# Kernel optimization log

Measured on AMD Instinct MI355X. Metric: run time of the kernel, lower is better.

Reference implementation:

```python
import jax, jax.numpy as jnp
import numpy as np

N_NODES = 100000
N_EDGES = 1600000
EPS = 1e-5  # nn.BatchNorm1d default eps


def setup_inputs() -> dict:
    key = jax.random.key(0)
    ks = jax.random.split(key, 6)
    x = jax.random.normal(ks[0], (N_NODES, 11), dtype=jnp.float32)
    edge_index = jax.random.randint(ks[1], (2, N_EDGES), 0, N_NODES, dtype=jnp.int64)
    edge_weight = jax.random.uniform(ks[2], (N_EDGES,), dtype=jnp.float32)
    W1 = jax.random.normal(ks[3], (11, 64), dtype=jnp.float32) * 0.3
    b1 = jnp.zeros((64,), dtype=jnp.float32)
    gamma = jnp.ones((64,), dtype=jnp.float32)
    beta = jnp.zeros((64,), dtype=jnp.float32)
    W2 = jax.random.normal(ks[4], (64, 128), dtype=jnp.float32) * 0.125
    b2 = jnp.zeros((128,), dtype=jnp.float32)
    return {"x": x, "edge_index": edge_index, "edge_weight": edge_weight,
            "W1": W1, "b1": b1, "gamma": gamma, "beta": beta, "W2": W2, "b2": b2}


def _gcn_conv(x, row, col, w, W, b, n_nodes):
    """PyG GCNConv: h = x @ W; symmetric-norm aggregate at col; + bias.
    row/col/w already include self loops (weight 1.0)."""
    h = x @ W  # [N, F_out]
    deg = jax.ops.segment_sum(w, col, num_segments=n_nodes)  # [N]
    dinv = jnp.where(deg > 0, jax.lax.rsqrt(jnp.maximum(deg, 1e-12)), 0.0)
    norm = dinv[row] * w * dinv[col]  # [E+N]
    msg = h[row] * norm[:, None]  # gather + scale, [E+N, F_out]
    out = jax.ops.segment_sum(msg, col, num_segments=n_nodes)  # scatter-add
    return out + b


def _batch_norm(x, gamma, beta):
    # training-mode BatchNorm1d over node dimension, biased variance
    mean = jnp.mean(x, axis=0)
    var = jnp.mean(jnp.square(x - mean), axis=0)
    return (x - mean) * jax.lax.rsqrt(var + EPS) * gamma + beta


def reference(x, edge_index, edge_weight, W1, b1, gamma, beta, W2, b2):
    n = x.shape[0]
    loops = jnp.arange(n, dtype=edge_index.dtype)
    row = jnp.concatenate([edge_index[0], loops])
    col = jnp.concatenate([edge_index[1], loops])
    w = jnp.concatenate([edge_weight, jnp.ones((n,), dtype=edge_weight.dtype)])

    h = _gcn_conv(x, row, col, w, W1, b1, n)
    h = _batch_norm(h, gamma, beta)
    h = jax.nn.relu(h)
    # dropout is identity at inference (deterministic baseline)
    out = _gcn_conv(h, row, col, w, W2, b2, n)
    return out
```

## Files before the change

kernel.cpp:

```cpp
#include <hip/hip_runtime.h>

#define F0 11
#define F1 64
#define F2 128
#define TN2 128

#define CHUNKS 64
#define BPR 12544
#define WPR (BPR / 2)
#define NBKT (CHUNKS * 8 * 4)
#define NN1 64

__device__ __forceinline__ unsigned short f2bf(float v) {
  unsigned u = __float_as_uint(v);
  unsigned r = u + 0x7FFFu + ((u >> 16) & 1u);
  return (unsigned short)(r >> 16);
}
__device__ __forceinline__ float bf2f(unsigned short s) {
  return __uint_as_float(((unsigned)s) << 16);
}
__device__ __forceinline__ float bf2f_lo(unsigned v) { return __uint_as_float(v << 16); }
__device__ __forceinline__ float bf2f_hi(unsigned v) { return __uint_as_float(v & 0xFFFF0000u); }

__global__ void k_pad(const float* __restrict__ x, unsigned short* __restrict__ x16b,
                      float* __restrict__ wdeg, int n) {
  int i = blockIdx.x * blockDim.x + threadIdx.x;
  if (i < n) wdeg[i] = 0.f;
  if (i >= n * 16) return;
  int r = i >> 4, f = i & 15;
  x16b[i] = (f < F0) ? f2bf(x[(size_t)r * F0 + f]) : (unsigned short)0;
}

__global__ __launch_bounds__(1024) void k_cnt8(const int* __restrict__ col,
                                               int* __restrict__ bcnt, int E, int CE) {
  __shared__ int scnt[16][8];
  int bid = blockIdx.x;
  int c = bid >> 2, q = bid & 3;
  int e0 = c * CE, e1 = min(E, e0 + CE);
  int S = (CE + 3) >> 2;
  int s0 = e0 + q * S, s1 = min(e1, s0 + S);
  int t = threadIdx.x, wv = t >> 6, lane = t & 63;
  int cr[8] = {0, 0, 0, 0, 0, 0, 0, 0};
  for (int e = s0 + t; e < s1; e += 1024) {
    int r = col[e] / BPR;
#pragma unroll
    for (int rr = 0; rr < 8; rr++) cr[rr] += (r == rr) ? 1 : 0;
  }
#pragma unroll
  for (int rr = 0; rr < 8; rr++) {
    int v = cr[rr];
#pragma unroll
    for (int d = 32; d > 0; d >>= 1) v += __shfl_down(v, d);
    if (lane == 0) scnt[wv][rr] = v;
  }
  __syncthreads();
  if (t < 8) {
    int s = 0;
    for (int i = 0; i < 16; i++) s += scnt[i][t];
    bcnt[(c * 8 + t) * 4 + q] = s;
  }
}

__global__ void k_scan8(const int* __restrict__ bcnt, int* __restrict__ boff) {
  __shared__ int s[1024];
  int t = threadIdx.x;
  int v0 = bcnt[2 * t], v1 = bcnt[2 * t + 1];
  int pv = v0 + v1;
  s[t] = pv;
  __syncthreads();
  for (int d = 1; d < 1024; d <<= 1) {
    int x = (t >= d) ? s[t - d] : 0;
    __syncthreads();
    s[t] += x;
    __syncthreads();
  }
  int ex = s[t] - pv;
  boff[2 * t] = ex;
  boff[2 * t + 1] = ex + v0;
  if (t == 1023) boff[2048] = s[1023];
}

__global__ __launch_bounds__(1024) void k_scatter(const int* __restrict__ col,
                                                  const int* __restrict__ row,
                                                  const float* __restrict__ w,
                                                  const int* __restrict__ boff,
                                                  unsigned short* __restrict__ bloc,
                                                  uint2* __restrict__ brw, int E, int CE) {
  __shared__ int cur[8];
  int bid = blockIdx.x;
  int c = bid >> 2, q = bid & 3;
  int t = threadIdx.x;
  if (t < 8) cur[t] = boff[(c * 8 + t) * 4 + q];
  __syncthreads();
  int e0 = c * CE, e1 = min(E, e0 + CE);
  int S = (CE + 3) >> 2;
  int s0 = e0 + q * S, s1 = min(e1, s0 + S);
  for (int e = s0 + t; e < s1; e += 1024) {
    int b = col[e];
    int r = b / BPR;
    int pos = atomicAdd(&cur[r], 1);
    bloc[pos] = (unsigned short)(b - r * BPR);
    brw[pos] = make_uint2((unsigned)row[e], __float_as_uint(w[e]));
  }
}

__global__ __launch_bounds__(1024) void k_hist2(const unsigned short* __restrict__ bloc,
                                                const uint2* __restrict__ brw,
                                                const int* __restrict__ boff,
                                                unsigned* __restrict__ partial,
                                                float* __restrict__ wdeg,
                                                int N, int ranges) {
  __shared__ unsigned lds[WPR];
  __shared__ float swdeg[BPR];
  int r = blockIdx.x % ranges;
  int c = blockIdx.x / ranges;
  int t = threadIdx.x;
  for (int i = t; i < WPR; i += 1024) lds[i] = 0;
  for (int i = t; i < BPR; i += 1024) swdeg[i] = 0.f;
  __syncthreads();
  int s0 = boff[(c * 8 + r) * 4], s1 = boff[(c * 8 + r) * 4 + 4];
  for (int i = s0 + t; i < s1; i += 1024) {
    int local = bloc[i];
    float wv = __uint_as_float(brw[i].y);
    atomicAdd(&lds[local >> 1], 1u << (16 * (local & 1)));
    atomicAdd(&swdeg[local], wv);
  }
  __syncthreads();
  unsigned* dst = partial + ((size_t)r * CHUNKS + c) * WPR;
  for (int i = t; i < WPR; i += 1024) dst[i] = lds[i];
  int lo = r * BPR;
  int hi = min(N, lo + BPR);
  for (int i = lo + t; i < hi; i += 1024) {
    float v = swdeg[i - lo];
    if (v != 0.f) atomicAdd(&wdeg[i], v);
  }
}

__global__ void k_dinv(const float* __restrict__ wdeg, float* __restrict__ dinv, int n) {
  int i = blockIdx.x * blockDim.x + threadIdx.x;
  if (i < n) dinv[i] = rsqrtf(1.0f + wdeg[i]);
}

__global__ void k_colprefix(const unsigned* __restrict__ partial,
                            unsigned short* __restrict__ rel,
                            int* __restrict__ cnt, int N, int npad) {
  int bin = blockIdx.x * blockDim.x + threadIdx.x;
  if (bin >= N) return;
  int r = bin / BPR, local = bin % BPR;
  int word = local >> 1, sh = 16 * (local & 1);
  const unsigned* p = partial + (size_t)r * CHUNKS * WPR + word;
  unsigned acc = 0;
  for (int c = 0; c < CHUNKS; c++) {
    unsigned v = (p[(size_t)c * WPR] >> sh) & 0xFFFFu;
    rel[(size_t)c * npad + bin] = (unsigned short)acc;
    acc += v;
  }
  cnt[bin] = (int)acc;
}

__global__ void k_scan1(const int* __restrict__ cnt, int* __restrict__ offs,
                        int* __restrict__ bsum, int n) {
  __shared__ int s[1024];
  int tid = threadIdx.x;
  int i = blockIdx.x * 1024 + tid;
  int v = (i < n) ? cnt[i] : 0;
  s[tid] = v;
  __syncthreads();
  for (int d = 1; d < 1024; d <<= 1) {
    int t = (tid >= d) ? s[tid - d] : 0;
    __syncthreads();
    s[tid] += t;
    __syncthreads();
  }
  if (i < n) offs[i] = s[tid] - v;
  if (tid == 1023) bsum[blockIdx.x] = s[1023];
}

__global__ void k_scan2(int* __restrict__ bsum, int nb) {
  __shared__ int s[256];
  __shared__ int carry;
  int t = threadIdx.x;
  if (t == 0) carry = 0;
  __syncthreads();
  for (int base = 0; base < nb; base += 256) {
    int v = (base + t < nb) ? bsum[base + t] : 0;
    s[t] = v;
    __syncthreads();
    for (int d = 1; d < 256; d <<= 1) {
      int x = (t >= d) ? s[t - d] : 0;
      __syncthreads();
      s[t] += x;
      __syncthreads();
    }
    int total = s[255];
    if (base + t < nb) bsum[base + t] = carry + s[t] - v;
    __syncthreads();
    if (t == 0) carry += total;
    __syncthreads();
  }
}

__global__ void k_scan3(int* __restrict__ offs, const int* __restrict__ bsum,
                        int n, int total) {
  int i = blockIdx.x * 1024 + threadIdx.x;
  if (i < n) offs[i] += bsum[blockIdx.x];
  if (i == 0) offs[n] = total;
}

__global__ __launch_bounds__(1024) void k_fill2(const unsigned short* __restrict__ bloc,
                                                const uint2* __restrict__ brw,
                                                const int* __restrict__ boff,
                                                const int* __restrict__ offs,
                                                const unsigned short* __restrict__ rel,
                                                const float* __restrict__ dinv,
                                                uint2* __restrict__ csr8,
                                                int N, int npad, int ranges) {
  __shared__ unsigned cur[WPR];
  int r = blockIdx.x % ranges;
  int c = blockIdx.x / ranges;
  int lo = r * BPR;
  int hi = min(N, lo + BPR);
  int t = threadIdx.x;
  const unsigned* rsrc = (const unsigned*)(rel + (size_t)c * npad + lo);
  int nw = (hi - lo + 1) >> 1;
  for (int i = t; i < nw; i += 1024) cur[i] = rsrc[i];
  __syncthreads();
  int s0 = boff[(c * 8 + r) * 4], s1 = boff[(c * 8 + r) * 4 + 4];
  for (int i = s0 + t; i < s1; i += 1024) {
    int local = bloc[i];
    int sh = 16 * (local & 1);
    unsigned old = atomicAdd(&cur[local >> 1], 1u << sh);
    unsigned myrel = (old >> sh) & 0xFFFFu;
    int pos = offs[lo + local] + (int)myrel;
    uint2 b = brw[i];
    float nm = dinv[b.x] * __uint_as_float(b.y);
    csr8[pos] = make_uint2(b.x | ((unsigned)local << 17), __float_as_uint(nm));
  }
}

__global__ __launch_bounds__(256) void k_agg1e(const unsigned short* __restrict__ x16b,
                                               const int* __restrict__ offs,
                                               const uint2* __restrict__ csr8,
                                               const float* __restrict__ dinv,
                                               const float* __restrict__ W1,
                                               const float* __restrict__ b1,
                                               unsigned short* __restrict__ h,
                                               float2* __restrict__ pbn, int N) {
  __shared__ float Ws[F0 * F1];
  __shared__ float bs[F1];
  __shared__ float sacc[NN1 * 16];
  __shared__ unsigned short sx[NN1 * 16];
  __shared__ float sdinv[NN1];
  __shared__ float sS[4][64], sQ[4][64];
  int t = threadIdx.x;
  int bid = blockIdx.x;
  int n0 = bid * NN1;
  int nn = min(NN1, N - n0);
  int lbase = n0 - (n0 / BPR) * BPR;
  for (int i = t; i < F0 * F1; i += 256) Ws[i] = W1[i];
  if (t < F1) bs[t] = b1[t];
  ((uint2*)sx)[t] = ((const uint2*)(x16b + (size_t)n0 * 16))[t];
  if (t < NN1) sdinv[t] = (t < nn) ? dinv[n0 + t] : 0.f;
  for (int i = t; i < NN1 * 16; i += 256) sacc[i] = 0.f;
  __syncthreads();
  int ebase = offs[n0], eend = offs[n0 + nn];
  int slot = t >> 4, f = t & 15;
  int nsub = (eend - ebase + 15) >> 4;
  int gs = ebase + slot * nsub;
  int ge = min(eend, gs + nsub);
  float sum = 0.f;
  int cid = -1;
  int e = gs;
  for (; e + 4 <= ge; e += 4) {
    uint2 v0 = csr8[e], v1 = csr8[e + 1], v2 = csr8[e + 2], v3 = csr8[e + 3];
    int i0 = (int)(v0.x >> 17) - lbase, i1 = (int)(v1.x >> 17) - lbase;
    int i2 = (int)(v2.x >> 17) - lbase, i3 = (int)(v3.x >> 17) - lbase;
    float c0 = __uint_as_float(v0.y) * bf2f(x16b[(size_t)(v0.x & 0x1FFFFu) * 16 + f]);
    float c1 = __uint_as_float(v1.y) * bf2f(x16b[(size_t)(v1.x & 0x1FFFFu) * 16 + f]);
    float c2 = __uint_as_float(v2.y) * bf2f(x16b[(size_t)(v2.x & 0x1FFFFu) * 16 + f]);
    float c3 = __uint_as_float(v3.y) * bf2f(x16b[(size_t)(v3.x & 0x1FFFFu) * 16 + f]);
    bool sm;
    sm = (i0 == cid); if (!sm && cid >= 0) atomicAdd(&sacc[cid * 16 + f], sum);
    sum = sm ? sum + c0 : c0; cid = i0;
    sm = (i1 == cid); if (!sm) atomicAdd(&sacc[cid * 16 + f], sum);
    sum = sm ? sum + c1 : c1; cid = i1;
    sm = (i2 == cid); if (!sm) atomicAdd(&sacc[cid * 16 + f], sum);
    sum = sm ? sum + c2 : c2; cid = i2;
    sm = (i3 == cid); if (!sm) atomicAdd(&sacc[cid * 16 + f], sum);
    sum = sm ? sum + c3 : c3; cid = i3;
  }
  for (; e < ge; e++) {
    uint2 v0 = csr8[e];
    int i0 = (int)(v0.x >> 17) - lbase;
    float c0 = __uint_as_float(v0.y) * bf2f(x16b[(size_t)(v0.x & 0x1FFFFu) * 16 + f]);
    bool sm = (i0 == cid);
    if (!sm && cid >= 0) atomicAdd(&sacc[cid * 16 + f], sum);
    sum = sm ? sum + c0 : c0; cid = i0;
  }
  if (cid >= 0) atomicAdd(&sacc[cid * 16 + f], sum);
  __syncthreads();
  for (int i = t; i < NN1 * 16; i += 256) {
    float di = sdinv[i >> 4];
    sacc[i] = di * (sacc[i] + di * bf2f(sx[i]));
  }
  __syncthreads();
  int ff = t & 63, wv = t >> 6;
  float S = 0.f, Q = 0.f;
  for (int i = 0; i < 16; i++) {
    int nd = wv + 4 * i;
    if (nd < nn) {
      float o = bs[ff];
#pragma unroll
      for (int k = 0; k < F0; k++) o += sacc[nd * 16 + k] * Ws[k * F1 + ff];
      h[(size_t)(n0 + nd) * F1 + ff] = f2bf(o);
      S += o; Q += o * o;
    }
  }
  sS[wv][ff] = S; sQ[wv][ff] = Q;
  __syncthreads();
  if (t < 64)
    pbn[(size_t)bid * 64 + t] =
        make_float2(sS[0][t] + sS[1][t] + sS[2][t] + sS[3][t],
                    sQ[0][t] + sQ[1][t] + sQ[2][t] + sQ[3][t]);
}

__global__ void k_bn_mid(const float2* __restrict__ pbn, float2* __restrict__ pbn2, int nrows) {
  __shared__ float sS[4][64], sQ[4][64];
  int t = threadIdx.x;
  int f = t & 63, g = t >> 6;
  int rpb = (nrows + 63) / 64;
  int b0 = blockIdx.x * rpb;
  int bend = min(nrows, b0 + rpb);
  float S = 0.f, Q = 0.f;
  for (int b = b0 + g; b < bend; b += 4) {
    float2 v = pbn[(size_t)b * 64 + f];
    S += v.x; Q += v.y;
  }
  sS[g][f] = S; sQ[g][f] = Q;
  __syncthreads();
  if (t < 64)
    pbn2[(size_t)blockIdx.x * 64 + t] =
        make_float2(sS[0][t] + sS[1][t] + sS[2][t] + sS[3][t],
                    sQ[0][t] + sQ[1][t] + sQ[2][t] + sQ[3][t]);
}

__global__ void k_bn_final(const float2* __restrict__ pbn2, const float* __restrict__ gamma,
                           const float* __restrict__ beta, float* __restrict__ scalef,
                           float* __restrict__ shiftf, int n) {
  __shared__ double sS[4][64], sQ[4][64];
  int t = threadIdx.x;
  int f = t & 63, g = t >> 6;
  double S = 0.0, Q = 0.0;
  for (int b = g; b < 64; b += 4) {
    float2 v = pbn2[(size_t)b * 64 + f];
    S += v.x; Q += v.y;
  }
  sS[g][f] = S; sQ[g][f] = Q;
  __syncthreads();
  if (t < 64) {
    double SS = sS[0][t] + sS[1][t] + sS[2][t] + sS[3][t];
    double QQ = sQ[0][t] + sQ[1][t] + sQ[2][t] + sQ[3][t];
    double mean = SS / (double)n;
    double var = QQ / (double)n - mean * mean;
    if (var < 0.0) var = 0.0;
    float scale = gamma[t] * (float)(1.0 / sqrt(var + 1e-5));
    scalef[t] = scale;
    shiftf[t] = beta[t] - (float)mean * scale;
  }
}

__global__ void k_hn(const unsigned short* __restrict__ h, const float* __restrict__ scalef,
                     const float* __restrict__ shiftf, unsigned short* __restrict__ hn,
                     int total4) {
  __shared__ float ssc[64], ssf[64];
  int t = threadIdx.x;
  if (t < 64) { ssc[t] = scalef[t]; ssf[t] = shiftf[t]; }
  __syncthreads();
  int idx = blockIdx.x * blockDim.x + t;
  int stride = gridDim.x * blockDim.x;
  const unsigned long long* hp = (const unsigned long long*)h;
  unsigned long long* hnp = (unsigned long long*)hn;
  for (int i = idx; i < total4; i += stride) {
    unsigned long long vv = hp[i];
    int f0 = (i * 4) & 63;
    float a = fmaxf(fmaf(bf2f_lo((unsigned)vv), ssc[f0 + 0], ssf[f0 + 0]), 0.f);
    float b = fmaxf(fmaf(bf2f_hi((unsigned)vv), ssc[f0 + 1], ssf[f0 + 1]), 0.f);
    float c = fmaxf(fmaf(bf2f_lo((unsigned)(vv >> 32)), ssc[f0 + 2], ssf[f0 + 2]), 0.f);
    float d = fmaxf(fmaf(bf2f_hi((unsigned)(vv >> 32)), ssc[f0 + 3], ssf[f0 + 3]), 0.f);
    hnp[i] = (unsigned long long)f2bf(a) | ((unsigned long long)f2bf(b) << 16) |
             ((unsigned long long)f2bf(c) << 32) | ((unsigned long long)f2bf(d) << 48);
  }
}

__global__ void k_agg2(const unsigned short* __restrict__ hn, const int* __restrict__ offs,
                       const uint2* __restrict__ csr8, const float* __restrict__ dinv,
                       unsigned short* __restrict__ agg2b, int n) {
  __shared__ unsigned s_soff[4][64];
  __shared__ float    s_nrm[4][64];
  int t = threadIdx.x;
  int wv = t >> 6;
  int lane = t & 63;
  int wid = (blockIdx.x * blockDim.x + t) >> 6;
  if (wid >= n) return;
  float di = dinv[wid];
  float a0 = di * bf2f(hn[(size_t)wid * F1 + lane]);
  float a1 = 0.f, a2 = 0.f, a3 = 0.f, a4 = 0.f, a5 = 0.f, a6 = 0.f, a7 = 0.f;
  int s = offs[wid], e = offs[wid + 1];
  for (int base = s; base < e; base += 64) {
    int m = e - base; if (m > 64) m = 64;
    if (lane < m) {
      uint2 v = csr8[base + lane];
      s_soff[wv][lane] = (v.x & 0x1FFFFu) * 64u;
      s_nrm[wv][lane] = __uint_as_float(v.y);
    } else {
      s_soff[wv][lane] = 0u;
      s_nrm[wv][lane] = 0.f;
    }
    int mp = (m + 7) & ~7;
    for (int j = 0; j < mp; j += 8) {
      unsigned o0 = s_soff[wv][j + 0], o1 = s_soff[wv][j + 1];
      unsigned o2 = s_soff[wv][j + 2], o3 = s_soff[wv][j + 3];
      unsigned o4 = s_soff[wv][j + 4], o5 = s_soff[wv][j + 5];
      unsigned o6 = s_soff[wv][j + 6], o7 = s_soff[wv][j + 7];
      float m0 = s_nrm[wv][j + 0], m1 = s_nrm[wv][j + 1];
      float m2 = s_nrm[wv][j + 2], m3 = s_nrm[wv][j + 3];
      float m4 = s_nrm[wv][j + 4], m5 = s_nrm[wv][j + 5];
      float m6 = s_nrm[wv][j + 6], m7 = s_nrm[wv][j + 7];
      a0 += m0 * bf2f(hn[(size_t)o0 + lane]);
      a1 += m1 * bf2f(hn[(size_t)o1 + lane]);
      a2 += m2 * bf2f(hn[(size_t)o2 + lane]);
      a3 += m3 * bf2f(hn[(size_t)o3 + lane]);
      a4 += m4 * bf2f(hn[(size_t)o4 + lane]);
      a5 += m5 * bf2f(hn[(size_t)o5 + lane]);
      a6 += m6 * bf2f(hn[(size_t)o6 + lane]);
      a7 += m7 * bf2f(hn[(size_t)o7 + lane]);
    }
  }
  float r = di * (((a0 + a1) + (a2 + a3)) + ((a4 + a5) + (a6 + a7)));
  agg2b[(size_t)wid * F1 + lane] = f2bf(r);
}

__global__ __launch_bounds__(256) void k_gemm2(const unsigned short* __restrict__ agg2b,
                                               const float* __restrict__ W2,
                                               const float* __restrict__ b2,
                                               float* __restrict__ out, int n) {
  __shared__ float Ws[F1 * F2];
  __shared__ float As[F1][TN2];
  int t = threadIdx.x;
  for (int i = t; i < F1 * F2 / 4; i += 256) ((float4*)Ws)[i] = ((const float4*)W2)[i];
  int nb = blockIdx.x * TN2;
  int node = t & 127;
  int kh = (t >> 7) * 32;
  int gnode = nb + node;
  if (gnode < n) {
    const uint4* src = (const uint4*)(agg2b + (size_t)gnode * F1 + kh);
#pragma unroll
    for (int j = 0; j < 4; j++) {
      uint4 v = src[j];
      As[kh + j * 8 + 0][node] = bf2f_lo(v.x);
      As[kh + j * 8 + 1][node] = bf2f_hi(v.x);
      As[kh + j * 8 + 2][node] = bf2f_lo(v.y);
      As[kh + j * 8 + 3][node] = bf2f_hi(v.y);
      As[kh + j * 8 + 4][node] = bf2f_lo(v.z);
      As[kh + j * 8 + 5][node] = bf2f_hi(v.z);
      As[kh + j * 8 + 6][node] = bf2f_lo(v.w);
      As[kh + j * 8 + 7][node] = bf2f_hi(v.w);
    }
  } else {
#pragma unroll
    for (int j = 0; j < 8; j++) {
      As[kh + j * 4 + 0][node] = 0.f;
      As[kh + j * 4 + 1][node] = 0.f;
      As[kh + j * 4 + 2][node] = 0.f;
      As[kh + j * 4 + 3][node] = 0.f;
    }
  }
  __syncthreads();

  int f0 = (t & 15) * 8;
  int n0 = (t >> 4) * 8;
  float acc[8][8];
  float bv[8];
#pragma unroll
  for (int j = 0; j < 8; j++) bv[j] = b2[f0 + j];
#pragma unroll
  for (int i = 0; i < 8; i++)
#pragma unroll
    for (int j = 0; j < 8; j++) acc[i][j] = bv[j];

#pragma unroll 4
  for (int k = 0; k < F1; k++) {
    float4 a0 = *(const float4*)&As[k][n0];
    float4 a1 = *(const float4*)&As[k][n0 + 4];
    float4 w0 = *(const float4*)&Ws[k * F2 + f0];
    float4 w1 = *(const float4*)&Ws[k * F2 + f0 + 4];
    float a[8] = {a0.x, a0.y, a0.z, a0.w, a1.x, a1.y, a1.z, a1.w};
    float w[8] = {w0.x, w0.y, w0.z, w0.w, w1.x, w1.y, w1.z, w1.w};
#pragma unroll
    for (int i = 0; i < 8; i++)
#pragma unroll
      for (int j = 0; j < 8; j++) acc[i][j] += a[i] * w[j];
  }

#pragma unroll
  for (int i = 0; i < 8; i++) {
    int gi = nb + n0 + i;
    if (gi < n) {
      float4 o0 = {acc[i][0], acc[i][1], acc[i][2], acc[i][3]};
      float4 o1 = {acc[i][4], acc[i][5], acc[i][6], acc[i][7]};
      *(float4*)&out[(size_t)gi * F2 + f0] = o0;
      *(float4*)&out[(size_t)gi * F2 + f0 + 4] = o1;
    }
  }
}

extern "C" void kernel_launch(void* const* d_in, const int* in_sizes, int n_in,
                              void* d_out, int out_size, void* d_ws, size_t ws_size,
                              hipStream_t stream) {
  const float* x     = (const float*)d_in[0];
  const int*   ei    = (const int*)d_in[1];
  const float* ew    = (const float*)d_in[2];
  const float* W1    = (const float*)d_in[3];
  const float* b1    = (const float*)d_in[4];
  const float* gamma = (const float*)d_in[5];
  const float* beta  = (const float*)d_in[6];
  const float* W2    = (const float*)d_in[7];
  const float* b2    = (const float*)d_in[8];
  float* out = (float*)d_out;

  int N = in_sizes[0] / F0;
  int E = in_sizes[1] / 2;
  const int* row = ei;
  const int* col = ei + E;
  if (N <= 0) return;

  int CE = (E + CHUNKS - 1) / CHUNKS;
  int RANGES = (N + BPR - 1) / BPR;
  int npad = RANGES * BPR;
  int NBLK = (N + NN1 - 1) / NN1;

  char* p = (char*)d_ws;
  auto alloc = [&](size_t bytes) -> void* {
    void* r = (void*)p;
    p += (bytes + 255) & ~(size_t)255;
    return r;
  };
  size_t partial_bytes = ((size_t)RANGES * CHUNKS * WPR * 4 + 255) & ~(size_t)255;
  size_t rel_bytes     = (size_t)CHUNKS * npad * 2;
  size_t h_bytes       = (size_t)N * F1 * 2;
  size_t region_bytes  = partial_bytes + rel_bytes;
  if (h_bytes > region_bytes) region_bytes = h_bytes;

  float*          dinv    = (float*)alloc((size_t)N * 4);
  float*          wdeg    = (float*)alloc((size_t)N * 4);
  int*            cnt     = (int*)alloc((size_t)N * 4);
  int*            offs    = (int*)alloc((size_t)(N + 1) * 4);
  int             NB      = (N + 1023) / 1024;
  int*            bsum    = (int*)alloc((size_t)NB * 4);
  uint2*          csr8    = (uint2*)alloc((size_t)E * 8);
  char*           region  = (char*)alloc(region_bytes);
  unsigned*       partial = (unsigned*)region;
  unsigned short* rel     = (unsigned short*)(region + partial_bytes);
  unsigned short* h       = (unsigned short*)region;
  unsigned short* x16b    = (unsigned short*)alloc((size_t)N * 16 * 2);
  unsigned short* hn      = (unsigned short*)alloc((size_t)N * F1 * 2);
  size_t bloc_bytes = (((size_t)E * 2) + 255) & ~(size_t)255;
  size_t bkt_bytes  = bloc_bytes + (size_t)E * 8;
  size_t a2b_bytes  = (size_t)N * F1 * 2;
  char*           bktreg  = (char*)alloc(bkt_bytes > a2b_bytes ? bkt_bytes : a2b_bytes);
  unsigned short* bloc    = (unsigned short*)bktreg;
  uint2*          brw     = (uint2*)(bktreg + bloc_bytes);
  unsigned short* agg2b   = (unsigned short*)bktreg;
  float2*         pbn     = (float2*)alloc((size_t)NBLK * 64 * 8);
  float2*         pbn2    = (float2*)alloc((size_t)64 * 64 * 8);
  float*          scalef  = (float*)alloc(64 * 4);
  float*          shiftf  = (float*)alloc(64 * 4);
  int*            bcnt    = (int*)alloc((size_t)NBKT * 4);
  int*            boff    = (int*)alloc((size_t)(NBKT + 1) * 4);
  (void)ws_size; (void)n_in; (void)out_size;

  int bW  = (N + 3) / 4;
  int bG2 = (N + TN2 - 1) / TN2;
  int gRC = CHUNKS * RANGES;

  k_pad<<<(N * 16 + 255) / 256, 256, 0, stream>>>(x, x16b, wdeg, N);
  k_cnt8<<<CHUNKS * 4, 1024, 0, stream>>>(col, bcnt, E, CE);
  k_scan8<<<1, 1024, 0, stream>>>(bcnt, boff);
  k_scatter<<<CHUNKS * 4, 1024, 0, stream>>>(col, row, ew, boff, bloc, brw, E, CE);
  k_hist2<<<gRC, 1024, 0, stream>>>(bloc, brw, boff, partial, wdeg, N, RANGES);
  k_dinv<<<(N + 255) / 256, 256, 0, stream>>>(wdeg, dinv, N);
  k_colprefix<<<(N + 255) / 256, 256, 0, stream>>>(partial, rel, cnt, N, npad);
  k_scan1<<<NB, 1024, 0, stream>>>(cnt, offs, bsum, N);
  k_scan2<<<1, 256, 0, stream>>>(bsum, NB);
  k_scan3<<<NB, 1024, 0, stream>>>(offs, bsum, N, E);
  k_fill2<<<gRC, 1024, 0, stream>>>(bloc, brw, boff, offs, rel, dinv, csr8, N, npad, RANGES);
  k_agg1e<<<NBLK, 256, 0, stream>>>(x16b, offs, csr8, dinv, W1, b1, h, pbn, N);
  k_bn_mid<<<64, 256, 0, stream>>>(pbn, pbn2, NBLK);
  k_bn_final<<<1, 256, 0, stream>>>(pbn2, gamma, beta, scalef, shiftf, N);
  k_hn<<<2048, 256, 0, stream>>>(h, scalef, shiftf, hn, N * F1 / 4);
  k_agg2<<<bW, 256, 0, stream>>>(hn, offs, csr8, dinv, agg2b, N);
  k_gemm2<<<bG2, 256, 0, stream>>>(agg2b, W2, b2, out, N);
}
```

Before: 212.2 us.

## Quantize normalized hidden features to uint8 for second aggregation

Tracks per-feature min/max alongside the batch-norm sums and derives one global scale from the post-ReLU maximum. The normalized activations are then stored as 8-bit unsigned integers instead of bf16, which halves the bytes gathered per edge in the second aggregation. The dinv kernel is also folded into the column-prefix kernel to drop one launch. The cost is a large loss of precision (256 levels shared across all features), which may break the accuracy tolerance.

```diff
diff --git a/kernel.cpp b/kernel.cpp
--- a/kernel.cpp
+++ b/kernel.cpp
@@ -136,14 +136,10 @@
   }
 }
 
-__global__ void k_dinv(const float* __restrict__ wdeg, float* __restrict__ dinv, int n) {
-  int i = blockIdx.x * blockDim.x + threadIdx.x;
-  if (i < n) dinv[i] = rsqrtf(1.0f + wdeg[i]);
-}
-
 __global__ void k_colprefix(const unsigned* __restrict__ partial,
                             unsigned short* __restrict__ rel,
-                            int* __restrict__ cnt, int N, int npad) {
+                            int* __restrict__ cnt, const float* __restrict__ wdeg,
+                            float* __restrict__ dinv, int N, int npad) {
   int bin = blockIdx.x * blockDim.x + threadIdx.x;
   if (bin >= N) return;
   int r = bin / BPR, local = bin % BPR;
@@ -156,6 +152,7 @@
     acc += v;
   }
   cnt[bin] = (int)acc;
+  dinv[bin] = rsqrtf(1.0f + wdeg[bin]);
 }
 
 __global__ void k_scan1(const int* __restrict__ cnt, int* __restrict__ offs,
@@ -245,13 +242,13 @@
                                                const float* __restrict__ W1,
                                                const float* __restrict__ b1,
                                                unsigned short* __restrict__ h,
-                                               float2* __restrict__ pbn, int N) {
+                                               float4* __restrict__ pbn, int N) {
   __shared__ float Ws[F0 * F1];
   __shared__ float bs[F1];
   __shared__ float sacc[NN1 * 16];
   __shared__ unsigned short sx[NN1 * 16];
   __shared__ float sdinv[NN1];
-  __shared__ float sS[4][64], sQ[4][64];
+  __shared__ float sS[4][64], sQ[4][64], sMn[4][64], sMx[4][64];
   int t = threadIdx.x;
   int bid = blockIdx.x;
   int n0 = bid * NN1;
@@ -305,7 +302,7 @@
   }
   __syncthreads();
   int ff = t & 63, wv = t >> 6;
-  float S = 0.f, Q = 0.f;
+  float S = 0.f, Q = 0.f, Mn = 1e30f, Mx = -1e30f;
   for (int i = 0; i < 16; i++) {
     int nd = wv + 4 * i;
     if (nd < nn) {
@@ -314,72 +311,96 @@
       for (int k = 0; k < F0; k++) o += sacc[nd * 16 + k] * Ws[k * F1 + ff];
       h[(size_t)(n0 + nd) * F1 + ff] = f2bf(o);
       S += o; Q += o * o;
+      Mn = fminf(Mn, o); Mx = fmaxf(Mx, o);
     }
   }
-  sS[wv][ff] = S; sQ[wv][ff] = Q;
+  sS[wv][ff] = S; sQ[wv][ff] = Q; sMn[wv][ff] = Mn; sMx[wv][ff] = Mx;
   __syncthreads();
   if (t < 64)
-    pbn[(size_t)bid * 64 + t] =
-        make_float2(sS[0][t] + sS[1][t] + sS[2][t] + sS[3][t],
-                    sQ[0][t] + sQ[1][t] + sQ[2][t] + sQ[3][t]);
-}
-
-__global__ void k_bn_mid(const float2* __restrict__ pbn, float2* __restrict__ pbn2, int nrows) {
-  __shared__ float sS[4][64], sQ[4][64];
+    pbn[(size_t)bid * 64 + t] = make_float4(
+        sS[0][t] + sS[1][t] + sS[2][t] + sS[3][t],
+        sQ[0][t] + sQ[1][t] + sQ[2][t] + sQ[3][t],
+        fminf(fminf(sMn[0][t], sMn[1][t]), fminf(sMn[2][t], sMn[3][t])),
+        fmaxf(fmaxf(sMx[0][t], sMx[1][t]), fmaxf(sMx[2][t], sMx[3][t])));
+}
+
+__global__ void k_bn_mid(const float4* __restrict__ pbn, float4* __restrict__ pbn2, int nrows) {
+  __shared__ float sS[4][64], sQ[4][64], sMn[4][64], sMx[4][64];
   int t = threadIdx.x;
   int f = t & 63, g = t >> 6;
   int rpb = (nrows + 63) / 64;
   int b0 = blockIdx.x * rpb;
   int bend = min(nrows, b0 + rpb);
-  float S = 0.f, Q = 0.f;
+  float S = 0.f, Q = 0.f, Mn = 1e30f, Mx = -1e30f;
   for (int b = b0 + g; b < bend; b += 4) {
-    float2 v = pbn[(size_t)b * 64 + f];
+    float4 v = pbn[(size_t)b * 64 + f];
     S += v.x; Q += v.y;
-  }
-  sS[g][f] = S; sQ[g][f] = Q;
+    Mn = fminf(Mn, v.z); Mx = fmaxf(Mx, v.w);
+  }
+  sS[g][f] = S; sQ[g][f] = Q; sMn[g][f] = Mn; sMx[g][f] = Mx;
   __syncthreads();
   if (t < 64)
-    pbn2[(size_t)blockIdx.x * 64 + t] =
-        make_float2(sS[0][t] + sS[1][t] + sS[2][t] + sS[3][t],
-                    sQ[0][t] + sQ[1][t] + sQ[2][t] + sQ[3][t]);
-}
-
-__global__ void k_bn_final(const float2* __restrict__ pbn2, const float* __restrict__ gamma,
+    pbn2[(size_t)blockIdx.x * 64 + t] = make_float4(
+        sS[0][t] + sS[1][t] + sS[2][t] + sS[3][t],
+        sQ[0][t] + sQ[1][t] + sQ[2][t] + sQ[3][t],
+        fminf(fminf(sMn[0][t], sMn[1][t]), fminf(sMn[2][t], sMn[3][t])),
+        fmaxf(fmaxf(sMx[0][t], sMx[1][t]), fmaxf(sMx[2][t], sMx[3][t])));
+}
+
+__global__ void k_bn_final(const float4* __restrict__ pbn2, const float* __restrict__ gamma,
                            const float* __restrict__ beta, float* __restrict__ scalef,
-                           float* __restrict__ shiftf, int n) {
+                           float* __restrict__ shiftf, float* __restrict__ qparams, int n) {
   __shared__ double sS[4][64], sQ[4][64];
+  __shared__ float sMn[4][64], sMx[4][64];
+  __shared__ float sM[64];
   int t = threadIdx.x;
   int f = t & 63, g = t >> 6;
   double S = 0.0, Q = 0.0;
+  float Mn = 1e30f, Mx = -1e30f;
   for (int b = g; b < 64; b += 4) {
-    float2 v = pbn2[(size_t)b * 64 + f];
+    float4 v = pbn2[(size_t)b * 64 + f];
     S += v.x; Q += v.y;
-  }
-  sS[g][f] = S; sQ[g][f] = Q;
+    Mn = fminf(Mn, v.z); Mx = fmaxf(Mx, v.w);
+  }
+  sS[g][f] = S; sQ[g][f] = Q; sMn[g][f] = Mn; sMx[g][f] = Mx;
   __syncthreads();
   if (t < 64) {
     double SS = sS[0][t] + sS[1][t] + sS[2][t] + sS[3][t];
     double QQ = sQ[0][t] + sQ[1][t] + sQ[2][t] + sQ[3][t];
+    float mn = fminf(fminf(sMn[0][t], sMn[1][t]), fminf(sMn[2][t], sMn[3][t]));
+    float mx = fmaxf(fmaxf(sMx[0][t], sMx[1][t]), fmaxf(sMx[2][t], sMx[3][t]));
     double mean = SS / (double)n;
     double var = QQ / (double)n - mean * mean;
     if (var < 0.0) var = 0.0;
     float scale = gamma[t] * (float)(1.0 / sqrt(var + 1e-5));
+    float shift = beta[t] - (float)mean * scale;
     scalef[t] = scale;
-    shiftf[t] = beta[t] - (float)mean * scale;
+    shiftf[t] = shift;
+    float hi = fmaxf(fmaxf(scale * mx + shift, scale * mn + shift), 0.f);
+    sM[t] = hi;
+  }
+  __syncthreads();
+  if (t == 0) {
+    float M = 0.f;
+    for (int i = 0; i < 64; i++) M = fmaxf(M, sM[i]);
+    float qs = (M > 1e-20f) ? 255.0f / M : 0.f;
+    qparams[0] = (M > 1e-20f) ? M / 255.0f : 0.f;
+    qparams[1] = qs;
   }
 }
 
 __global__ void k_hn(const unsigned short* __restrict__ h, const float* __restrict__ scalef,
-                     const float* __restrict__ shiftf, unsigned short* __restrict__ hn,
-                     int total4) {
+                     const float* __restrict__ shiftf, const float* __restrict__ qparams,
+                     unsigned char* __restrict__ hn8, int total4) {
   __shared__ float ssc[64], ssf[64];
   int t = threadIdx.x;
   if (t < 64) { ssc[t] = scalef[t]; ssf[t] = shiftf[t]; }
   __syncthreads();
+  float qs = qparams[1];
   int idx = blockIdx.x * blockDim.x + t;
   int stride = gridDim.x * blockDim.x;
   const unsigned long long* hp = (const unsigned long long*)h;
-  unsigned long long* hnp = (unsigned long long*)hn;
+  unsigned* hnp = (unsigned*)hn8;
   for (int i = idx; i < total4; i += stride) {
     unsigned long long vv = hp[i];
     int f0 = (i * 4) & 63;
@@ -387,13 +408,17 @@
     float b = fmaxf(fmaf(bf2f_hi((unsigned)vv), ssc[f0 + 1], ssf[f0 + 1]), 0.f);
     float c = fmaxf(fmaf(bf2f_lo((unsigned)(vv >> 32)), ssc[f0 + 2], ssf[f0 + 2]), 0.f);
     float d = fmaxf(fmaf(bf2f_hi((unsigned)(vv >> 32)), ssc[f0 + 3], ssf[f0 + 3]), 0.f);
-    hnp[i] = (unsigned long long)f2bf(a) | ((unsigned long long)f2bf(b) << 16) |
-             ((unsigned long long)f2bf(c) << 32) | ((unsigned long long)f2bf(d) << 48);
-  }
-}
-
-__global__ void k_agg2(const unsigned short* __restrict__ hn, const int* __restrict__ offs,
+    unsigned ua = min(255u, (unsigned)(a * qs + 0.5f));
+    unsigned ub = min(255u, (unsigned)(b * qs + 0.5f));
+    unsigned uc = min(255u, (unsigned)(c * qs + 0.5f));
+    unsigned ud = min(255u, (unsigned)(d * qs + 0.5f));
+    hnp[i] = ua | (ub << 8) | (uc << 16) | (ud << 24);
+  }
+}
+
+__global__ void k_agg2(const unsigned char* __restrict__ hn8, const int* __restrict__ offs,
                        const uint2* __restrict__ csr8, const float* __restrict__ dinv,
+                       const float* __restrict__ qparams,
                        unsigned short* __restrict__ agg2b, int n) {
   __shared__ unsigned s_soff[4][64];
   __shared__ float    s_nrm[4][64];
@@ -402,8 +427,9 @@
   int lane = t & 63;
   int wid = (blockIdx.x * blockDim.x + t) >> 6;
   if (wid >= n) return;
+  float sd = qparams[0];
   float di = dinv[wid];
-  float a0 = di * bf2f(hn[(size_t)wid * F1 + lane]);
+  float a0 = di * sd * (float)hn8[(size_t)wid * F1 + lane];
   float a1 = 0.f, a2 = 0.f, a3 = 0.f, a4 = 0.f, a5 = 0.f, a6 = 0.f, a7 = 0.f;
   int s = offs[wid], e = offs[wid + 1];
   for (int base = s; base < e; base += 64) {
@@ -411,7 +437,7 @@
     if (lane < m) {
       uint2 v = csr8[base + lane];
       s_soff[wv][lane] = (v.x & 0x1FFFFu) * 64u;
-      s_nrm[wv][lane] = __uint_as_float(v.y);
+      s_nrm[wv][lane] = sd * __uint_as_float(v.y);
     } else {
       s_soff[wv][lane] = 0u;
       s_nrm[wv][lane] = 0.f;
@@ -426,14 +452,14 @@
       float m2 = s_nrm[wv][j + 2], m3 = s_nrm[wv][j + 3];
       float m4 = s_nrm[wv][j + 4], m5 = s_nrm[wv][j + 5];
       float m6 = s_nrm[wv][j + 6], m7 = s_nrm[wv][j + 7];
-      a0 += m0 * bf2f(hn[(size_t)o0 + lane]);
-      a1 += m1 * bf2f(hn[(size_t)o1 + lane]);
-      a2 += m2 * bf2f(hn[(size_t)o2 + lane]);
-      a3 += m3 * bf2f(hn[(size_t)o3 + lane]);
-      a4 += m4 * bf2f(hn[(size_t)o4 + lane]);
-      a5 += m5 * bf2f(hn[(size_t)o5 + lane]);
-      a6 += m6 * bf2f(hn[(size_t)o6 + lane]);
-      a7 += m7 * bf2f(hn[(size_t)o7 + lane]);
+      a0 += m0 * (float)hn8[(size_t)o0 + lane];
+      a1 += m1 * (float)hn8[(size_t)o1 + lane];
+      a2 += m2 * (float)hn8[(size_t)o2 + lane];
+      a3 += m3 * (float)hn8[(size_t)o3 + lane];
+      a4 += m4 * (float)hn8[(size_t)o4 + lane];
+      a5 += m5 * (float)hn8[(size_t)o5 + lane];
+      a6 += m6 * (float)hn8[(size_t)o6 + lane];
+      a7 += m7 * (float)hn8[(size_t)o7 + lane];
     }
   }
   float r = di * (((a0 + a1) + (a2 + a3)) + ((a4 + a5) + (a6 + a7)));
@@ -563,7 +589,7 @@
   unsigned short* rel     = (unsigned short*)(region + partial_bytes);
   unsigned short* h       = (unsigned short*)region;
   unsigned short* x16b    = (unsigned short*)alloc((size_t)N * 16 * 2);
-  unsigned short* hn      = (unsigned short*)alloc((size_t)N * F1 * 2);
+  unsigned char*  hn8     = (unsigned char*)alloc((size_t)N * F1);
   size_t bloc_bytes = (((size_t)E * 2) + 255) & ~(size_t)255;
   size_t bkt_bytes  = bloc_bytes + (size_t)E * 8;
   size_t a2b_bytes  = (size_t)N * F1 * 2;
@@ -571,10 +597,11 @@
   unsigned short* bloc    = (unsigned short*)bktreg;
   uint2*          brw     = (uint2*)(bktreg + bloc_bytes);
   unsigned short* agg2b   = (unsigned short*)bktreg;
-  float2*         pbn     = (float2*)alloc((size_t)NBLK * 64 * 8);
-  float2*         pbn2    = (float2*)alloc((size_t)64 * 64 * 8);
+  float4*         pbn     = (float4*)alloc((size_t)NBLK * 64 * 16);
+  float4*         pbn2    = (float4*)alloc((size_t)64 * 64 * 16);
   float*          scalef  = (float*)alloc(64 * 4);
   float*          shiftf  = (float*)alloc(64 * 4);
+  float*          qparams = (float*)alloc(2 * 4);
   int*            bcnt    = (int*)alloc((size_t)NBKT * 4);
   int*            boff    = (int*)alloc((size_t)(NBKT + 1) * 4);
   (void)ws_size; (void)n_in; (void)out_size;
@@ -588,16 +615,15 @@
   k_scan8<<<1, 1024, 0, stream>>>(bcnt, boff);
   k_scatter<<<CHUNKS * 4, 1024, 0, stream>>>(col, row, ew, boff, bloc, brw, E, CE);
   k_hist2<<<gRC, 1024, 0, stream>>>(bloc, brw, boff, partial, wdeg, N, RANGES);
-  k_dinv<<<(N + 255) / 256, 256, 0, stream>>>(wdeg, dinv, N);
-  k_colprefix<<<(N + 255) / 256, 256, 0, stream>>>(partial, rel, cnt, N, npad);
+  k_colprefix<<<(N + 255) / 256, 256, 0, stream>>>(partial, rel, cnt, wdeg, dinv, N, npad);
   k_scan1<<<NB, 1024, 0, stream>>>(cnt, offs, bsum, N);
   k_scan2<<<1, 256, 0, stream>>>(bsum, NB);
   k_scan3<<<NB, 1024, 0, stream>>>(offs, bsum, N, E);
   k_fill2<<<gRC, 1024, 0, stream>>>(bloc, brw, boff, offs, rel, dinv, csr8, N, npad, RANGES);
   k_agg1e<<<NBLK, 256, 0, stream>>>(x16b, offs, csr8, dinv, W1, b1, h, pbn, N);
   k_bn_mid<<<64, 256, 0, stream>>>(pbn, pbn2, NBLK);
-  k_bn_final<<<1, 256, 0, stream>>>(pbn2, gamma, beta, scalef, shiftf, N);
-  k_hn<<<2048, 256, 0, stream>>>(h, scalef, shiftf, hn, N * F1 / 4);
-  k_agg2<<<bW, 256, 0, stream>>>(hn, offs, csr8, dinv, agg2b, N);
+  k_bn_final<<<1, 256, 0, stream>>>(pbn2, gamma, beta, scalef, shiftf, qparams, N);
+  k_hn<<<2048, 256, 0, stream>>>(h, scalef, shiftf, qparams, hn8, N * F1 / 4);
+  k_agg2<<<bW, 256, 0, stream>>>(hn8, offs, csr8, dinv, qparams, agg2b, N);
   k_gemm2<<<bG2, 256, 0, stream>>>(agg2b, W2, b2, out, N);
 }
```

Measured after the change: 211.1 us. Within noise of the previous version (-0.5%).
